# Optimization experiments

Measured on AMD Instinct MI355X. Metric: run time of the kernel, lower is better.

## Reference

```python
import jax, jax.numpy as jnp
import numpy as np

# dims: R ranks, B batch, HQ q-heads, HKV kv-heads-per-rank, G = HQ//HKV group size,
# D head dim, S kv splits (hardcoded 32 in module), L max kv len per rank, P pages per rank
R, B, HQ, HKV, D, S, L, P = 4, 16, 32, 2, 128, 32, 2048, 32768
G = HQ // HKV  # kv_group_num = num_q_heads // num_kv_heads_per_rank
NEG = -jnp.inf


def setup_inputs() -> dict:
    key = jax.random.key(0)
    k1, k2, k3, k4, k5 = jax.random.split(key, 5)
    q = jax.random.normal(k1, (B, HQ, D), jnp.float32)
    k_cache = jax.random.normal(k2, (R, P, HKV, D), jnp.float32)
    v_cache = jax.random.normal(k3, (R, P, HKV, D), jnp.float32)
    block_table = jax.random.randint(k4, (R, B, L), 0, P, jnp.int32)
    # per-rank kv lengths; min 64 to keep all math well-defined
    kv_lens_per_rank = jax.random.randint(k5, (R, B), 64, L + 1, jnp.int32)
    return dict(q=q, k_cache=k_cache, v_cache=v_cache,
                block_table=block_table, kv_lens_per_rank=kv_lens_per_rank)


def _attend(q, k_cache, v_cache, block_table, kv_lens):
    scale = D ** -0.5
    # page_size == 1: block_table entries are token slots in the per-rank cache.
    ridx = jnp.arange(R)[:, None, None]
    k = k_cache[ridx, block_table]  # [R,B,L,HKV,D]
    v = v_cache[ridx, block_table]  # [R,B,L,HKV,D]

    # GQA: q head h uses local kv head h // G on each rank
    qg = q.reshape(B, HKV, G, D)
    scores = jnp.einsum('bkgd,rblkd->rbkgl', qg, k) * scale  # [R,B,HKV,G,L]

    n = jnp.arange(L)
    valid = n[None, None, :] < kv_lens[..., None]            # [R,B,L]
    scores = jnp.where(valid[:, :, None, None, :], scores, NEG)

    # stage 1: split-KV. split s covers [s*per, (s+1)*per) with per = ceil(len/S)
    per = -(-kv_lens // S)                                   # [R,B]
    sid = n[None, None, :] // per[..., None]                 # [R,B,L]

    lse_s = []
    for s in range(S):  # fixed small loop over NUM_KV_SPLITS
        m = jnp.where((sid == s)[:, :, None, None, :], scores, NEG)
        lse_s.append(jax.scipy.special.logsumexp(m, axis=-1))  # [R,B,HKV,G]
    lse_s = jnp.stack(lse_s)  # [S,R,B,HKV,G]; empty splits -> -inf (kernel skips them)

    # stage 2: local combine over splits. NOTE (faithful to kernel): local_out stores
    # the UNNORMALIZED accumulator sum_s exp(lse_s - m_r) * o_s together with
    # lse_r = m_r + log(sum_s exp(lse_s - m_r)), where m_r = max_s lse_s.
    m_r = jnp.max(lse_s, axis=0)                              # [R,B,HKV,G]
    lse_r = m_r + jnp.log(jnp.sum(jnp.exp(lse_s - m_r), axis=0))
    # sum_s exp(lse_s - m_r) * (softmax_s @ v_s) == sum_n exp(score_n - m_r) * v_n
    p = jnp.exp(scores - m_r[..., None])                      # masked entries -> 0
    acc_r = jnp.einsum('rbkgl,rblkd->rbkgd', p, v)            # [R,B,HKV,G,D]

    acc = acc_r.reshape(R, B, HQ, D)
    lse = lse_r.reshape(R, B, HQ)

    # stage 3: global lse-weighted combine across ranks (online softmax == this)
    M = jnp.max(lse, axis=0)                                  # [B,HQ]
    w = jnp.exp(lse - M)                                      # [R,B,HQ]
    out = jnp.sum(w[..., None] * acc, axis=0) / jnp.sum(w, axis=0)[..., None]
    return out  # [B,HQ,D]


def reference(q, k_cache, v_cache, block_table, kv_lens_per_rank):
    return _attend(q, k_cache, v_cache, block_table, kv_lens_per_rank)
```

## Files before the change

### kernel.cpp

```cpp
#include <hip/hip_runtime.h>
#include <math.h>

#define R_ 4
#define B_ 16
#define HQ_ 32
#define HKV_ 2
#define G_ 16
#define D_ 128
#define S_ 32
#define L_ 2048
#define P_ 32768
#define TS_ 64
#define KSTR 136
#define PSTR 18
#define NEGINF (-INFINITY)

typedef _Float16 h2 __attribute__((ext_vector_type(2)));
typedef _Float16 h4 __attribute__((ext_vector_type(4)));
typedef _Float16 h8 __attribute__((ext_vector_type(8)));

#if defined(__has_builtin)
#  if __has_builtin(__builtin_amdgcn_fdot2)
#    define FDOT2(a,b,c) __builtin_amdgcn_fdot2((a),(b),(c),false)
#  endif
#endif
#ifndef FDOT2
static __device__ __forceinline__ float fdot2_sw(h2 a, h2 b, float c) {
  return c + (float)a.x*(float)b.x + (float)a.y*(float)b.y;
}
#  define FDOT2(a,b,c) fdot2_sw((a),(b),(c))
#endif


__global__ __launch_bounds__(256, 6) void fd_stage1(
    const float* __restrict__ q, const float* __restrict__ kc,
    const float* __restrict__ vc, const int* __restrict__ bt,
    const int* __restrict__ lens,
    float* __restrict__ lse_split, float* __restrict__ chunk_m,
    _Float16* __restrict__ chunk_acc)
{
  const int t   = threadIdx.x;
  const int blk = blockIdx.x;
  const int s   = blk & 31;
  const int hkv = (blk >> 5) & 1;
  const int b   = (blk >> 6) & 15;
  const int r   = blk >> 10;

  const int len = lens[r*B_ + b];
  const int per = (len + 31) >> 5;
  const int n0  = s*per;
  const int tn  = min(per, len - n0);

  float* lse_out = lse_split + ((r*B_ + b)*HKV_ + hkv)*(S_*G_);
  const int cmbase = (((r*B_ + b)*HKV_ + hkv)*S_ + s)*G_;
  _Float16* ca = chunk_acc + (size_t)(((r*B_ + b)*HKV_ + hkv)*S_ + s)*(G_*D_);

  if (tn <= 0) {
    if (t < G_) { lse_out[s*G_ + t] = NEGINF; chunk_m[cmbase + t] = NEGINF; }
    h8 z = {(_Float16)0,(_Float16)0,(_Float16)0,(_Float16)0,
            (_Float16)0,(_Float16)0,(_Float16)0,(_Float16)0};
    *(h8*)&ca[t*8] = z;
    return;
  }

  __shared__ _Float16 q_s[G_][KSTR];
  __shared__ _Float16 k_s[TS_][KSTR];
  __shared__ float    p_s[TS_][PSTR];

  {
    const float* qb = q + (b*HQ_ + hkv*G_)*D_;
    int f4 = t;
    #pragma unroll
    for (int i = 0; i < 2; ++i, f4 += 256) {
      const int g = f4 >> 5, dd = (f4 & 31)*4;
      const float4 v = *(const float4*)&qb[g*D_ + dd];
      h4 hv; hv.x=(_Float16)v.x; hv.y=(_Float16)v.y; hv.z=(_Float16)v.z; hv.w=(_Float16)v.w;
      *(h4*)&q_s[g][dd] = hv;
    }
  }

  const int* btb   = bt + (r*B_ + b)*L_;
  const int kvbase = r*(P_*HKV_*D_) + hkv*D_;

  {
    const int lane = t & 31, rw = t >> 5;
    for (int row = rw; row < tn; row += 8) {
      const int pg = btb[n0 + row];
      const float4 v = *(const float4*)&kc[kvbase + pg*(HKV_*D_) + lane*4];
      h4 hv; hv.x=(_Float16)v.x; hv.y=(_Float16)v.y; hv.z=(_Float16)v.z; hv.w=(_Float16)v.w;
      *(h4*)&k_s[row][lane*4] = hv;
    }
  }
  __syncthreads();

  const int sg = t >> 4, nl = t & 15;
  const int KN = (tn + 15) >> 4;
  float s0 = 0.f, s1 = 0.f, s2 = 0.f, s3 = 0.f;
  #pragma unroll 4
  for (int d8 = 0; d8 < 16; ++d8) {
    const h8 q8 = *(const h8*)&q_s[sg][d8*8];
    const h8 k0 = *(const h8*)&k_s[nl][d8*8];
    #pragma unroll
    for (int j = 0; j < 4; ++j) s0 = FDOT2(((const h2*)&q8)[j], ((const h2*)&k0)[j], s0);
    if (KN > 1) {
      const h8 k1 = *(const h8*)&k_s[nl + 16][d8*8];
      #pragma unroll
      for (int j = 0; j < 4; ++j) s1 = FDOT2(((const h2*)&q8)[j], ((const h2*)&k1)[j], s1);
    }
    if (KN > 2) {
      const h8 k2 = *(const h8*)&k_s[nl + 32][d8*8];
      #pragma unroll
      for (int j = 0; j < 4; ++j) s2 = FDOT2(((const h2*)&q8)[j], ((const h2*)&k2)[j], s2);
    }
    if (KN > 3) {
      const h8 k3 = *(const h8*)&k_s[nl + 48][d8*8];
      #pragma unroll
      for (int j = 0; j < 4; ++j) s3 = FDOT2(((const h2*)&q8)[j], ((const h2*)&k3)[j], s3);
    }
  }
  const float sc = 0.08838834764831845f;
  const float sv0 = (nl      < tn) ? s0*sc : NEGINF;
  const float sv1 = (nl + 16 < tn) ? s1*sc : NEGINF;
  const float sv2 = (nl + 32 < tn) ? s2*sc : NEGINF;
  const float sv3 = (nl + 48 < tn) ? s3*sc : NEGINF;

  float pm = fmaxf(fmaxf(sv0, sv1), fmaxf(sv2, sv3));
  #pragma unroll
  for (int off = 1; off < 16; off <<= 1) pm = fmaxf(pm, __shfl_xor(pm, off));
  float ps = __expf(sv0 - pm) + __expf(sv1 - pm) + __expf(sv2 - pm) + __expf(sv3 - pm);
  #pragma unroll
  for (int off = 1; off < 16; off <<= 1) ps += __shfl_xor(ps, off);

  if (nl == 0) {
    lse_out[s*G_ + sg] = pm + __logf(ps);
    chunk_m[cmbase + sg] = pm;
  }

  p_s[nl][sg] = __expf(sv0 - pm);
  if (KN > 1) p_s[nl + 16][sg] = __expf(sv1 - pm);
  if (KN > 2) p_s[nl + 32][sg] = __expf(sv2 - pm);
  if (KN > 3) p_s[nl + 48][sg] = __expf(sv3 - pm);
  __syncthreads();

  const int d4 = (t & 31)*4;
  const int g2 = (t >> 5)*2;
  float4 a0 = make_float4(0.f,0.f,0.f,0.f);
  float4 a1 = make_float4(0.f,0.f,0.f,0.f);
  #pragma unroll 4
  for (int n = 0; n < tn; ++n) {
    const int pg = btb[n0 + n];
    const float4 v4 = *(const float4*)&vc[kvbase + pg*(HKV_*D_) + d4];
    const float2 pp = *(const float2*)&p_s[n][g2];
    a0.x += pp.x*v4.x; a0.y += pp.x*v4.y; a0.z += pp.x*v4.z; a0.w += pp.x*v4.w;
    a1.x += pp.y*v4.x; a1.y += pp.y*v4.y; a1.z += pp.y*v4.z; a1.w += pp.y*v4.w;
  }

  h4 o0; o0.x=(_Float16)a0.x; o0.y=(_Float16)a0.y; o0.z=(_Float16)a0.z; o0.w=(_Float16)a0.w;
  h4 o1; o1.x=(_Float16)a1.x; o1.y=(_Float16)a1.y; o1.z=(_Float16)a1.z; o1.w=(_Float16)a1.w;
  *(h4*)&ca[g2*D_ + d4]       = o0;
  *(h4*)&ca[(g2 + 1)*D_ + d4] = o1;
}

__global__ __launch_bounds__(128) void fd_stage2(
    const float* __restrict__ lse_split, const float* __restrict__ chunk_m,
    const _Float16* __restrict__ chunk_acc, float* __restrict__ out)
{
  const int bh  = blockIdx.x;
  const int b   = bh >> 5, h = bh & 31;
  const int hkv = h >> 4, g = h & 15;
  const int d   = threadIdx.x;

  float m_r[R_], lse_r[R_];
  #pragma unroll
  for (int r = 0; r < R_; ++r) {
    const float* ls = lse_split + ((r*B_ + b)*HKV_ + hkv)*(S_*G_) + g;
    float m = NEGINF;
    #pragma unroll 8
    for (int s2 = 0; s2 < S_; ++s2) m = fmaxf(m, ls[s2*G_]);
    float sum = 0.f;
    #pragma unroll 8
    for (int s2 = 0; s2 < S_; ++s2) sum += __expf(ls[s2*G_] - m);
    m_r[r]   = m;
    lse_r[r] = m + __logf(sum);
  }
  const float M = fmaxf(fmaxf(lse_r[0], lse_r[1]), fmaxf(lse_r[2], lse_r[3]));
  float denom = 0.f, o = 0.f;
  #pragma unroll
  for (int r = 0; r < R_; ++r) {
    const float w = __expf(lse_r[r] - M);
    denom += w;
    const float* cm = chunk_m + (((r*B_ + b)*HKV_ + hkv)*S_)*G_ + g;
    const _Float16* ca = chunk_acc
        + (size_t)(((r*B_ + b)*HKV_ + hkv)*S_)*(G_*D_) + g*D_ + d;
    float a = 0.f;
    #pragma unroll 8
    for (int c = 0; c < S_; ++c)
      a += __expf(cm[c*G_] - m_r[r]) * (float)ca[(size_t)c*(G_*D_)];
    o += w * a;
  }
  out[(size_t)bh*D_ + d] = o / denom;
}

extern "C" void kernel_launch(void* const* d_in, const int* in_sizes, int n_in,
                              void* d_out, int out_size, void* d_ws, size_t ws_size,
                              hipStream_t stream) {
  const float* q   = (const float*)d_in[0];
  const float* kc  = (const float*)d_in[1];
  const float* vc  = (const float*)d_in[2];
  const int*   bt  = (const int*)d_in[3];
  const int*   len = (const int*)d_in[4];
  float* out = (float*)d_out;
  float* ws  = (float*)d_ws;

  const size_t lse_f = (size_t)R_*B_*HKV_*S_*G_;
  float*    lse_split = ws;
  float*    chunk_m   = ws + lse_f;
  _Float16* chunk_acc = (_Float16*)(ws + 2*lse_f);

  fd_stage1<<<dim3(R_*B_*HKV_*S_), dim3(256), 0, stream>>>(
      q, kc, vc, bt, len, lse_split, chunk_m, chunk_acc);
  fd_stage2<<<dim3(B_*HQ_), dim3(128), 0, stream>>>(
      lse_split, chunk_m, chunk_acc, out);
}
```

Baseline: 307.7 us.

## Use MFMA for QK and PV in split-KV stage with staged transposed V

Replaces the fdot2-based QK scores and scalar PV accumulation in stage 1 with 16x16x32 f16 MFMA instructions. V rows are now gathered into a transposed fp16 shared tile up front, alongside K, with page indices cached in shared memory. Softmax max and sum are reduced across four waves through shared memory. The chunk accumulator layout changes to D-major, and stage 2 is updated to match. Shared memory per block grows and the occupancy hint drops from 6 to 3. P is also rounded to fp16 before the PV product, which adds some rounding error.

New measurement: 325.4 us. 5.8% more time.

```diff
diff --git a/kernel.cpp b/kernel.cpp
--- a/kernel.cpp
+++ b/kernel.cpp
@@ -12,27 +12,17 @@
 #define P_ 32768
 #define TS_ 64
 #define KSTR 136
-#define PSTR 18
+#define VSTR 72
 #define NEGINF (-INFINITY)
+#define SENT (-1e30f)
 
 typedef _Float16 h2 __attribute__((ext_vector_type(2)));
 typedef _Float16 h4 __attribute__((ext_vector_type(4)));
 typedef _Float16 h8 __attribute__((ext_vector_type(8)));
-
-#if defined(__has_builtin)
-#  if __has_builtin(__builtin_amdgcn_fdot2)
-#    define FDOT2(a,b,c) __builtin_amdgcn_fdot2((a),(b),(c),false)
-#  endif
-#endif
-#ifndef FDOT2
-static __device__ __forceinline__ float fdot2_sw(h2 a, h2 b, float c) {
-  return c + (float)a.x*(float)b.x + (float)a.y*(float)b.y;
-}
-#  define FDOT2(a,b,c) fdot2_sw((a),(b),(c))
-#endif
-
-
-__global__ __launch_bounds__(256, 6) void fd_stage1(
+typedef float    f4v __attribute__((ext_vector_type(4)));
+
+
+__global__ __launch_bounds__(256, 3) void fd_stage1(
     const float* __restrict__ q, const float* __restrict__ kc,
     const float* __restrict__ vc, const int* __restrict__ bt,
     const int* __restrict__ lens,
@@ -51,114 +41,151 @@
   const int n0  = s*per;
   const int tn  = min(per, len - n0);
 
-  float* lse_out = lse_split + ((r*B_ + b)*HKV_ + hkv)*(S_*G_);
+  float* lse_out   = lse_split + ((r*B_ + b)*HKV_ + hkv)*(S_*G_);
   const int cmbase = (((r*B_ + b)*HKV_ + hkv)*S_ + s)*G_;
-  _Float16* ca = chunk_acc + (size_t)(((r*B_ + b)*HKV_ + hkv)*S_ + s)*(G_*D_);
+  _Float16* ca2 = chunk_acc + (size_t)(((r*B_ + b)*HKV_ + hkv)*S_ + s)*(D_*G_);
 
   if (tn <= 0) {
     if (t < G_) { lse_out[s*G_ + t] = NEGINF; chunk_m[cmbase + t] = NEGINF; }
     h8 z = {(_Float16)0,(_Float16)0,(_Float16)0,(_Float16)0,
             (_Float16)0,(_Float16)0,(_Float16)0,(_Float16)0};
-    *(h8*)&ca[t*8] = z;
+    ((h8*)ca2)[t] = z;
     return;
   }
 
-  __shared__ _Float16 q_s[G_][KSTR];
-  __shared__ _Float16 k_s[TS_][KSTR];
-  __shared__ float    p_s[TS_][PSTR];
+  __shared__ __align__(16) _Float16 q_s[G_][KSTR];
+  __shared__ __align__(16) _Float16 k_s[TS_][KSTR];
+  __shared__ __align__(16) _Float16 v2_sT[D_][VSTR];
+  __shared__ __align__(16) _Float16 p2_sT[G_][VSTR];
+  __shared__ float red_m[4][G_];
+  __shared__ float red_s[4][G_];
+  __shared__ int   page_s[TS_];
+
+  const int* btb   = bt + (r*B_ + b)*L_;
+  const int kvbase = r*(P_*HKV_*D_) + hkv*D_;
+
+  if (t < TS_) page_s[t] = (t < tn) ? btb[n0 + t] : 0;
+  __syncthreads();
+
+  {
+    const int lane32 = t & 31, r0 = t >> 5;
+    #pragma unroll
+    for (int it = 0; it < 8; ++it) {
+      const int row = r0 + 8*it;
+      if (row < tn) {
+        const float4 v = *(const float4*)&kc[kvbase + page_s[row]*(HKV_*D_) + lane32*4];
+        h4 hv; hv.x=(_Float16)v.x; hv.y=(_Float16)v.y; hv.z=(_Float16)v.z; hv.w=(_Float16)v.w;
+        *(h4*)&k_s[row][lane32*4] = hv;
+      }
+    }
+  }
+
+  {
+    const int d2  = t & 63;
+    const int rg0 = t >> 6;
+    #pragma unroll
+    for (int it = 0; it < 4; ++it) {
+      const int row = (rg0 + 4*it)*4;
+      float2 v0 = make_float2(0.f,0.f), v1 = v0, v2 = v0, v3 = v0;
+      if (row     < tn) v0 = *(const float2*)&vc[kvbase + page_s[row  ]*(HKV_*D_) + 2*d2];
+      if (row + 1 < tn) v1 = *(const float2*)&vc[kvbase + page_s[row+1]*(HKV_*D_) + 2*d2];
+      if (row + 2 < tn) v2 = *(const float2*)&vc[kvbase + page_s[row+2]*(HKV_*D_) + 2*d2];
+      if (row + 3 < tn) v3 = *(const float2*)&vc[kvbase + page_s[row+3]*(HKV_*D_) + 2*d2];
+      h4 a; a.x=(_Float16)v0.x; a.y=(_Float16)v1.x; a.z=(_Float16)v2.x; a.w=(_Float16)v3.x;
+      h4 c; c.x=(_Float16)v0.y; c.y=(_Float16)v1.y; c.z=(_Float16)v2.y; c.w=(_Float16)v3.y;
+      *(h4*)&v2_sT[2*d2    ][row] = a;
+      *(h4*)&v2_sT[2*d2 + 1][row] = c;
+    }
+  }
 
   {
     const float* qb = q + (b*HQ_ + hkv*G_)*D_;
-    int f4 = t;
-    #pragma unroll
-    for (int i = 0; i < 2; ++i, f4 += 256) {
-      const int g = f4 >> 5, dd = (f4 & 31)*4;
+    int f4i = t;
+    #pragma unroll
+    for (int i = 0; i < 2; ++i, f4i += 256) {
+      const int g = f4i >> 5, dd = (f4i & 31)*4;
       const float4 v = *(const float4*)&qb[g*D_ + dd];
       h4 hv; hv.x=(_Float16)v.x; hv.y=(_Float16)v.y; hv.z=(_Float16)v.z; hv.w=(_Float16)v.w;
       *(h4*)&q_s[g][dd] = hv;
     }
   }
-
-  const int* btb   = bt + (r*B_ + b)*L_;
-  const int kvbase = r*(P_*HKV_*D_) + hkv*D_;
-
-  {
-    const int lane = t & 31, rw = t >> 5;
-    for (int row = rw; row < tn; row += 8) {
-      const int pg = btb[n0 + row];
-      const float4 v = *(const float4*)&kc[kvbase + pg*(HKV_*D_) + lane*4];
-      h4 hv; hv.x=(_Float16)v.x; hv.y=(_Float16)v.y; hv.z=(_Float16)v.z; hv.w=(_Float16)v.w;
-      *(h4*)&k_s[row][lane*4] = hv;
-    }
-  }
-  __syncthreads();
-
-  const int sg = t >> 4, nl = t & 15;
-  const int KN = (tn + 15) >> 4;
-  float s0 = 0.f, s1 = 0.f, s2 = 0.f, s3 = 0.f;
-  #pragma unroll 4
-  for (int d8 = 0; d8 < 16; ++d8) {
-    const h8 q8 = *(const h8*)&q_s[sg][d8*8];
-    const h8 k0 = *(const h8*)&k_s[nl][d8*8];
-    #pragma unroll
-    for (int j = 0; j < 4; ++j) s0 = FDOT2(((const h2*)&q8)[j], ((const h2*)&k0)[j], s0);
-    if (KN > 1) {
-      const h8 k1 = *(const h8*)&k_s[nl + 16][d8*8];
-      #pragma unroll
-      for (int j = 0; j < 4; ++j) s1 = FDOT2(((const h2*)&q8)[j], ((const h2*)&k1)[j], s1);
-    }
-    if (KN > 2) {
-      const h8 k2 = *(const h8*)&k_s[nl + 32][d8*8];
-      #pragma unroll
-      for (int j = 0; j < 4; ++j) s2 = FDOT2(((const h2*)&q8)[j], ((const h2*)&k2)[j], s2);
-    }
-    if (KN > 3) {
-      const h8 k3 = *(const h8*)&k_s[nl + 48][d8*8];
-      #pragma unroll
-      for (int j = 0; j < 4; ++j) s3 = FDOT2(((const h2*)&q8)[j], ((const h2*)&k3)[j], s3);
-    }
-  }
+  __syncthreads();
+
+  const int w    = t >> 6;
+  const int lane = t & 63;
+  const int ln   = lane & 15;
+  const int quad = lane >> 4;
+  const int nrow = w*16 + ln;
+
+  f4v acc = {0.f, 0.f, 0.f, 0.f};
+  #pragma unroll
+  for (int ks = 0; ks < 4; ++ks) {
+    const h8 af = *(const h8*)&q_s[ln][ks*32 + quad*8];
+    const h8 bf = *(const h8*)&k_s[nrow][ks*32 + quad*8];
+    acc = __builtin_amdgcn_mfma_f32_16x16x32_f16(af, bf, acc, 0, 0, 0);
+  }
+
   const float sc = 0.08838834764831845f;
-  const float sv0 = (nl      < tn) ? s0*sc : NEGINF;
-  const float sv1 = (nl + 16 < tn) ? s1*sc : NEGINF;
-  const float sv2 = (nl + 32 < tn) ? s2*sc : NEGINF;
-  const float sv3 = (nl + 48 < tn) ? s3*sc : NEGINF;
-
-  float pm = fmaxf(fmaxf(sv0, sv1), fmaxf(sv2, sv3));
-  #pragma unroll
-  for (int off = 1; off < 16; off <<= 1) pm = fmaxf(pm, __shfl_xor(pm, off));
-  float ps = __expf(sv0 - pm) + __expf(sv1 - pm) + __expf(sv2 - pm) + __expf(sv3 - pm);
-  #pragma unroll
-  for (int off = 1; off < 16; off <<= 1) ps += __shfl_xor(ps, off);
-
-  if (nl == 0) {
-    lse_out[s*G_ + sg] = pm + __logf(ps);
-    chunk_m[cmbase + sg] = pm;
-  }
-
-  p_s[nl][sg] = __expf(sv0 - pm);
-  if (KN > 1) p_s[nl + 16][sg] = __expf(sv1 - pm);
-  if (KN > 2) p_s[nl + 32][sg] = __expf(sv2 - pm);
-  if (KN > 3) p_s[nl + 48][sg] = __expf(sv3 - pm);
-  __syncthreads();
-
-  const int d4 = (t & 31)*4;
-  const int g2 = (t >> 5)*2;
-  float4 a0 = make_float4(0.f,0.f,0.f,0.f);
-  float4 a1 = make_float4(0.f,0.f,0.f,0.f);
-  #pragma unroll 4
-  for (int n = 0; n < tn; ++n) {
-    const int pg = btb[n0 + n];
-    const float4 v4 = *(const float4*)&vc[kvbase + pg*(HKV_*D_) + d4];
-    const float2 pp = *(const float2*)&p_s[n][g2];
-    a0.x += pp.x*v4.x; a0.y += pp.x*v4.y; a0.z += pp.x*v4.z; a0.w += pp.x*v4.w;
-    a1.x += pp.y*v4.x; a1.y += pp.y*v4.y; a1.z += pp.y*v4.z; a1.w += pp.y*v4.w;
-  }
-
-  h4 o0; o0.x=(_Float16)a0.x; o0.y=(_Float16)a0.y; o0.z=(_Float16)a0.z; o0.w=(_Float16)a0.w;
-  h4 o1; o1.x=(_Float16)a1.x; o1.y=(_Float16)a1.y; o1.z=(_Float16)a1.z; o1.w=(_Float16)a1.w;
-  *(h4*)&ca[g2*D_ + d4]       = o0;
-  *(h4*)&ca[(g2 + 1)*D_ + d4] = o1;
+  const bool vld = (nrow < tn);
+  float sv[4], pm[4];
+  #pragma unroll
+  for (int i = 0; i < 4; ++i) { sv[i] = vld ? acc[i]*sc : SENT; pm[i] = sv[i]; }
+  #pragma unroll
+  for (int off = 1; off < 16; off <<= 1) {
+    #pragma unroll
+    for (int i = 0; i < 4; ++i) pm[i] = fmaxf(pm[i], __shfl_xor(pm[i], off));
+  }
+  float ts[4];
+  #pragma unroll
+  for (int i = 0; i < 4; ++i) ts[i] = __expf(sv[i] - pm[i]);
+  #pragma unroll
+  for (int off = 1; off < 16; off <<= 1) {
+    #pragma unroll
+    for (int i = 0; i < 4; ++i) ts[i] += __shfl_xor(ts[i], off);
+  }
+  if (ln == 0) {
+    #pragma unroll
+    for (int i = 0; i < 4; ++i) {
+      red_m[w][quad*4 + i] = pm[i];
+      red_s[w][quad*4 + i] = ts[i];
+    }
+  }
+  __syncthreads();
+
+  float pmg[4];
+  #pragma unroll
+  for (int i = 0; i < 4; ++i) {
+    const int hd = quad*4 + i;
+    const float m0 = red_m[0][hd], m1 = red_m[1][hd];
+    const float m2 = red_m[2][hd], m3 = red_m[3][hd];
+    const float mg = fmaxf(fmaxf(m0, m1), fmaxf(m2, m3));
+    pmg[i] = mg;
+    if (w == 0 && ln == 0) {
+      const float ps = red_s[0][hd]*__expf(m0 - mg) + red_s[1][hd]*__expf(m1 - mg)
+                     + red_s[2][hd]*__expf(m2 - mg) + red_s[3][hd]*__expf(m3 - mg);
+      lse_out[s*G_ + hd]  = mg + __logf(ps);
+      chunk_m[cmbase + hd] = mg;
+    }
+  }
+  #pragma unroll
+  for (int i = 0; i < 4; ++i)
+    p2_sT[quad*4 + i][nrow] = (_Float16)__expf(sv[i] - pmg[i]);
+  __syncthreads();
+
+  const int KS2 = (tn + 31) >> 5;
+  f4v o0 = {0.f,0.f,0.f,0.f}, o1 = {0.f,0.f,0.f,0.f};
+  const int dc0 = (2*w)*16 + ln, dc1 = (2*w + 1)*16 + ln;
+  for (int ks = 0; ks < KS2; ++ks) {
+    const h8 pa  = *(const h8*)&p2_sT[ln][ks*32 + quad*8];
+    const h8 vb0 = *(const h8*)&v2_sT[dc0][ks*32 + quad*8];
+    const h8 vb1 = *(const h8*)&v2_sT[dc1][ks*32 + quad*8];
+    o0 = __builtin_amdgcn_mfma_f32_16x16x32_f16(pa, vb0, o0, 0, 0, 0);
+    o1 = __builtin_amdgcn_mfma_f32_16x16x32_f16(pa, vb1, o1, 0, 0, 0);
+  }
+  h4 w0; w0.x=(_Float16)o0[0]; w0.y=(_Float16)o0[1]; w0.z=(_Float16)o0[2]; w0.w=(_Float16)o0[3];
+  h4 w1; w1.x=(_Float16)o1[0]; w1.y=(_Float16)o1[1]; w1.z=(_Float16)o1[2]; w1.w=(_Float16)o1[3];
+  *(h4*)&ca2[dc0*G_ + quad*4] = w0;
+  *(h4*)&ca2[dc1*G_ + quad*4] = w1;
 }
 
 __global__ __launch_bounds__(128) void fd_stage2(
@@ -191,11 +218,11 @@
     denom += w;
     const float* cm = chunk_m + (((r*B_ + b)*HKV_ + hkv)*S_)*G_ + g;
     const _Float16* ca = chunk_acc
-        + (size_t)(((r*B_ + b)*HKV_ + hkv)*S_)*(G_*D_) + g*D_ + d;
+        + (size_t)(((r*B_ + b)*HKV_ + hkv)*S_)*(D_*G_) + d*G_ + g;
     float a = 0.f;
     #pragma unroll 8
     for (int c = 0; c < S_; ++c)
-      a += __expf(cm[c*G_] - m_r[r]) * (float)ca[(size_t)c*(G_*D_)];
+      a += __expf(cm[c*G_] - m_r[r]) * (float)ca[(size_t)c*(D_*G_)];
     o += w * a;
   }
   out[(size_t)bh*D_ + d] = o / denom;
```
